# Performance work log

Measured on AMD Instinct MI355X. Metric: run time of the kernel, lower is better.

Reference implementation:

```python
import jax, jax.numpy as jnp
import numpy as np

B, T, V, D, H, C = 64, 512, 50000, 128, 256, 50


def setup_inputs() -> dict:
    key = jax.random.key(0)
    ks = jax.random.split(key, 15)
    s = 0.05
    rn = lambda k, shape: jax.random.normal(k, shape, jnp.float32) * s
    words = jax.random.randint(ks[0], (B, T), 0, V)
    target = jax.random.randint(ks[1], (B, T), 0, C)
    seq_len = jax.random.randint(ks[2], (B,), T // 2, T + 1)
    seq_len = seq_len.at[0].set(T)  # ensure at least one full-length sequence
    return dict(
        words=words, target=target, seq_len=seq_len,
        emb=rn(ks[3], (V, D)),
        W_ih_f=rn(ks[4], (4 * H, D)), W_hh_f=rn(ks[5], (4 * H, H)), b_f=rn(ks[6], (4 * H,)),
        W_ih_b=rn(ks[7], (4 * H, D)), W_hh_b=rn(ks[8], (4 * H, H)), b_b=rn(ks[9], (4 * H,)),
        fc_W=rn(ks[10], (C, 2 * H)), fc_b=rn(ks[11], (C,)),
        trans=rn(ks[12], (C, C)), start_s=rn(ks[13], (C,)), end_s=rn(ks[14], (C,)),
    )


def _lstm(x, W_ih, W_hh, b):
    # unidirectional LSTM, PyTorch gate order (i, f, g, o). x: [B,T,D] -> h: [B,T,H]
    Hh = W_hh.shape[1]
    xg = jnp.einsum('btd,gd->btg', x, W_ih) + b  # [B,T,4H]

    def step(carry, xt):
        h, c = carry
        g = xt + h @ W_hh.T
        i, f, gg, o = jnp.split(g, 4, axis=-1)
        c = jax.nn.sigmoid(f) * c + jax.nn.sigmoid(i) * jnp.tanh(gg)
        h = jax.nn.sigmoid(o) * jnp.tanh(c)
        return (h, c), h

    h0 = jnp.zeros((x.shape[0], Hh), x.dtype)
    _, hs = jax.lax.scan(step, (h0, h0), jnp.swapaxes(xg, 0, 1))
    return jnp.swapaxes(hs, 0, 1)


def _rev_idx(seq_len, t_len):
    # per-sequence time-reversal indices (packed-sequence semantics for the backward LSTM)
    t = jnp.arange(t_len)[None, :]
    L = seq_len[:, None]
    return jnp.where(t < L, L - 1 - t, t)


def _bilstm_crf_loss(words, target, seq_len, emb, W_ih_f, W_hh_f, b_f,
                     W_ih_b, W_hh_b, b_b, fc_W, fc_b, trans, start_s, end_s):
    x = emb[words]  # [B,T,D]
    h_f = _lstm(x, W_ih_f, W_hh_f, b_f)
    idx = _rev_idx(seq_len, x.shape[1])
    x_rev = jnp.take_along_axis(x, idx[:, :, None], axis=1)
    h_b = jnp.take_along_axis(_lstm(x_rev, W_ih_b, W_hh_b, b_b), idx[:, :, None], axis=1)
    feats = jnp.concatenate([h_f, h_b], axis=-1) @ fc_W.T + fc_b  # [B,T,C]
    logits = jax.nn.log_softmax(feats, axis=-1)
    mask = jnp.arange(x.shape[1])[None, :] < seq_len[:, None]  # [B,T] bool

    # --- CRF normalizer (forward algorithm) ---
    alpha0 = logits[:, 0] + start_s  # [B,C]

    def step(alpha, inp):
        emit_t, m_t = inp  # [B,C], [B]
        tmp = alpha[:, :, None] + trans[None, :, :] + emit_t[:, None, :]
        new = jax.nn.logsumexp(tmp, axis=1)
        return jnp.where(m_t[:, None], new, alpha), None

    alpha, _ = jax.lax.scan(step, alpha0,
                            (jnp.swapaxes(logits, 0, 1)[1:], jnp.swapaxes(mask, 0, 1)[1:]))
    norm = jax.nn.logsumexp(alpha + end_s, axis=1)  # [B]

    # --- gold path score ---
    maskf = mask.astype(logits.dtype)
    emit = jnp.take_along_axis(logits, target[:, :, None], axis=2)[..., 0]  # [B,T]
    trans_sc = trans[target[:, :-1], target[:, 1:]]  # [B,T-1]
    last = target[jnp.arange(target.shape[0]), seq_len - 1]
    gold = (emit * maskf).sum(1) + (trans_sc * maskf[:, 1:]).sum(1) \
           + start_s[target[:, 0]] + end_s[last]

    return jnp.mean(norm - gold)


def reference(words, target, seq_len, emb, W_ih_f, W_hh_f, b_f,
              W_ih_b, W_hh_b, b_b, fc_W, fc_b, trans, start_s, end_s):
    return _bilstm_crf_loss(words, target, seq_len, emb, W_ih_f, W_hh_f, b_f,
                            W_ih_b, W_hh_b, b_b, fc_W, fc_b, trans, start_s, end_s)
```

## Files before the change

kernel.cpp:

```cpp
#include <hip/hip_runtime.h>
#include <hip/hip_bf16.h>

#define BB 64
#define TT 512
#define DD 128
#define HH 256
#define G4 1024
#define CC 50

typedef __bf16 bf16x8 __attribute__((ext_vector_type(8)));
typedef float  f32x4  __attribute__((ext_vector_type(4)));
typedef _Float16 h16x2 __attribute__((ext_vector_type(2)));

#if defined(__has_builtin)
#if __has_builtin(__builtin_amdgcn_fdot2)
#define HAS_FDOT2 1
#endif
#endif

__device__ __forceinline__ float bl16(unsigned u) { return __uint_as_float(u << 16); }
__device__ __forceinline__ float bh16(unsigned u) { return __uint_as_float(u & 0xffff0000u); }

__device__ __forceinline__ float sigf(float x) {
    return 1.f / (1.f + __expf(-x));
}
__device__ __forceinline__ float tanh_s(float x) {
    float ax = fabsf(x);
    float e = __expf(-2.f * ax);
    float r = (1.f - e) / (1.f + e);
    return copysignf(r, x);
}

__device__ __forceinline__ float dot8(float acc, uint4 w, uint4 h) {
#ifdef HAS_FDOT2
    acc = __builtin_amdgcn_fdot2(__builtin_bit_cast(h16x2, w.x),
                                 __builtin_bit_cast(h16x2, h.x), acc, false);
    acc = __builtin_amdgcn_fdot2(__builtin_bit_cast(h16x2, w.y),
                                 __builtin_bit_cast(h16x2, h.y), acc, false);
    acc = __builtin_amdgcn_fdot2(__builtin_bit_cast(h16x2, w.z),
                                 __builtin_bit_cast(h16x2, h.z), acc, false);
    acc = __builtin_amdgcn_fdot2(__builtin_bit_cast(h16x2, w.w),
                                 __builtin_bit_cast(h16x2, h.w), acc, false);
#else
    {
        h16x2 a = __builtin_bit_cast(h16x2, w.x), b = __builtin_bit_cast(h16x2, h.x);
        acc = fmaf((float)a.x, (float)b.x, acc); acc = fmaf((float)a.y, (float)b.y, acc);
        a = __builtin_bit_cast(h16x2, w.y); b = __builtin_bit_cast(h16x2, h.y);
        acc = fmaf((float)a.x, (float)b.x, acc); acc = fmaf((float)a.y, (float)b.y, acc);
        a = __builtin_bit_cast(h16x2, w.z); b = __builtin_bit_cast(h16x2, h.z);
        acc = fmaf((float)a.x, (float)b.x, acc); acc = fmaf((float)a.y, (float)b.y, acc);
        a = __builtin_bit_cast(h16x2, w.w); b = __builtin_bit_cast(h16x2, h.w);
        acc = fmaf((float)a.x, (float)b.x, acc); acc = fmaf((float)a.y, (float)b.y, acc);
    }
#endif
    return acc;
}

__global__ __launch_bounds__(256) void k_cvt(
    const float* __restrict__ src, __hip_bfloat16* __restrict__ dst, int n)
{
    int i = (blockIdx.x * 256 + threadIdx.x) * 8;
    if (i + 8 <= n) {
        float4 a = *(const float4*)(src + i);
        float4 b = *(const float4*)(src + i + 4);
        __hip_bfloat16 o[8];
        o[0] = __float2bfloat16(a.x); o[1] = __float2bfloat16(a.y);
        o[2] = __float2bfloat16(a.z); o[3] = __float2bfloat16(a.w);
        o[4] = __float2bfloat16(b.x); o[5] = __float2bfloat16(b.y);
        o[6] = __float2bfloat16(b.z); o[7] = __float2bfloat16(b.w);
        *(uint4*)(dst + i) = *(const uint4*)o;
    }
}

__global__ __launch_bounds__(256) void k_pack(
    const float* __restrict__ Wf, const float* __restrict__ Wb,
    uint4* __restrict__ Wp)
{
    int blk = blockIdx.x;
    int g   = blk & 3;
    int kc  = (blk >> 2) & 31;
    int dir = blk >> 7;
    int j = threadIdx.x;
    int row = g * 256 + j;
    const float* src = (dir ? Wb : Wf) + (size_t)row * 256 + kc * 8;
    float4 a = *(const float4*)src;
    float4 b = *(const float4*)(src + 4);
    _Float16 o[8];
    o[0] = (_Float16)a.x; o[1] = (_Float16)a.y;
    o[2] = (_Float16)a.z; o[3] = (_Float16)a.w;
    o[4] = (_Float16)b.x; o[5] = (_Float16)b.y;
    o[6] = (_Float16)b.z; o[7] = (_Float16)b.w;
    Wp[((size_t)(dir * 32 + kc) * 4 + g) * 256 + j] = *(const uint4*)o;
}

__global__ __launch_bounds__(256, 2) void k_xg(
    const int* __restrict__ words,
    const float* __restrict__ embf,
    const __hip_bfloat16* __restrict__ Wih,
    const float* __restrict__ bfv, const float* __restrict__ bbv,
    __hip_bfloat16* __restrict__ xg)
{
    __shared__ __align__(16) __hip_bfloat16 A[64][136];
    int tid = threadIdx.x;
    int bt0 = blockIdx.x * 64;

    {
        int r = tid >> 2;
        int c0 = (tid & 3) * 32;
        int word = words[bt0 + r];
        const float* src = embf + (size_t)word * DD + c0;
#pragma unroll
        for (int i = 0; i < 8; ++i) {
            float4 v = *(const float4*)(src + i * 4);
            __hip_bfloat16 o[4] = {__float2bfloat16(v.x), __float2bfloat16(v.y),
                                   __float2bfloat16(v.z), __float2bfloat16(v.w)};
            *(uint2*)&A[r][c0 + i * 4] = *(const uint2*)o;
        }
    }
    __syncthreads();

    int wave = tid >> 6, lane = tid & 63;
    int m = lane & 15, quad = lane >> 4;

    bf16x8 afr[4][4];
#pragma unroll
    for (int ms = 0; ms < 4; ++ms)
#pragma unroll
        for (int kf = 0; kf < 4; ++kf)
            afr[ms][kf] = *(const bf16x8*)&A[ms * 16 + m][quad * 8 + kf * 32];

#pragma unroll 1
    for (int i = 0; i < 32; ++i) {
        int nt = wave * 32 + i;
        int gate_g = nt * 16 + m;
        int dir = gate_g >> 10;
        int gate = gate_g & 1023;
        const __hip_bfloat16* brow = Wih + (size_t)gate_g * DD + quad * 8;
        bf16x8 bfr[4];
#pragma unroll
        for (int kf = 0; kf < 4; ++kf) bfr[kf] = *(const bf16x8*)(brow + kf * 32);
        float bv = dir ? bbv[gate] : bfv[gate];
        size_t dbase = (size_t)dir * (size_t)(BB * TT * G4);

#pragma unroll
        for (int ms = 0; ms < 4; ++ms) {
            f32x4 acc = {0.f, 0.f, 0.f, 0.f};
#pragma unroll
            for (int kf = 0; kf < 4; ++kf)
                acc = __builtin_amdgcn_mfma_f32_16x16x32_bf16(afr[ms][kf], bfr[kf], acc, 0, 0, 0);
#pragma unroll
            for (int r = 0; r < 4; ++r) {
                int btrow = bt0 + ms * 16 + quad * 4 + r;
                xg[dbase + (size_t)btrow * G4 + gate] = __float2bfloat16(acc[r] + bv);
            }
        }
    }
}

__global__ __launch_bounds__(512)
__attribute__((amdgpu_waves_per_eu(2, 2)))
void k_lstm(
    const __hip_bfloat16* __restrict__ xg,
    const uint4* __restrict__ Wp,
    const int* __restrict__ seq_len,
    __hip_bfloat16* __restrict__ hcat)
{
    int b = blockIdx.x & 63;
    int dir = blockIdx.x >> 6;
    int tid = threadIdx.x;
    int j   = tid & 255;
    int half = tid >> 8;

    __shared__ __align__(16) uint4 wlds[16 * 512];
    __shared__ __align__(16) _Float16 hbf[2][HH];
    __shared__ float pbuf[4][HH];

    const uint4* Wd = Wp + (size_t)dir * (32 * 4 * 256);

    uint4 wr[12][4];
#pragma unroll
    for (int kcl = 0; kcl < 12; ++kcl)
#pragma unroll
        for (int g = 0; g < 4; ++g)
            wr[kcl][g] = Wd[(((kcl + 16 * half) * 4 + g) * 256) + j];

#pragma unroll
    for (int kcl = 12; kcl < 16; ++kcl)
#pragma unroll
        for (int g = 0; g < 4; ++g)
            wlds[((kcl - 12) * 4 + g) * 512 + tid] =
                Wd[(((kcl + 16 * half) * 4 + g) * 256) + j];

    if (half == 0) hbf[0][j] = (_Float16)0.f;
    float c = 0.f;
    int L = seq_len[b];
    const __hip_bfloat16* xgb = xg + (size_t)dir * (size_t)(BB * TT * G4)
                                   + (size_t)b * TT * G4;

    int tc = dir ? (L - 1) : 0;
    float xv0 = 0.f, xv1 = 0.f, xv2 = 0.f, xv3 = 0.f;
    if (half == 0) {
        const __hip_bfloat16* xr = xgb + (size_t)tc * G4 + j;
        xv0 = __bfloat162float(xr[0]);   xv1 = __bfloat162float(xr[256]);
        xv2 = __bfloat162float(xr[512]); xv3 = __bfloat162float(xr[768]);
    }
    __syncthreads();

#pragma unroll 1
    for (int t = 0; t < TT; ++t) {
#pragma unroll
        for (int kcl = 0; kcl < 12; ++kcl)
#pragma unroll
            for (int g = 0; g < 4; ++g)
                asm volatile("" : "+v"(wr[kcl][g].x), "+v"(wr[kcl][g].y),
                                  "+v"(wr[kcl][g].z), "+v"(wr[kcl][g].w));

        int cur = t & 1, nxt = cur ^ 1;
        int tn = t + 1;
        int tcn = dir ? ((tn < L) ? (L - 1 - tn) : tn) : tn;
        bool pf = (tn < TT);
        __hip_bfloat16 p0, p1, p2, p3;
        if (half == 0 && pf) {
            const __hip_bfloat16* xr = xgb + (size_t)tcn * G4 + j;
            p0 = xr[0]; p1 = xr[256]; p2 = xr[512]; p3 = xr[768];
        }

        unsigned off = 0;
        asm volatile("" : "+v"(off));

        const _Float16* hrow = &hbf[cur][half * 128];
        float a0 = 0.f, a1 = 0.f, a2 = 0.f, a3 = 0.f;
#pragma unroll
        for (int kcl = 0; kcl < 12; ++kcl) {
            uint4 hv = *(const uint4*)(hrow + kcl * 8);
            a0 = dot8(a0, wr[kcl][0], hv);
            a1 = dot8(a1, wr[kcl][1], hv);
            a2 = dot8(a2, wr[kcl][2], hv);
            a3 = dot8(a3, wr[kcl][3], hv);
        }
#pragma unroll
        for (int kcl = 12; kcl < 16; ++kcl) {
            uint4 hv = *(const uint4*)(hrow + kcl * 8);
            int m0 = (kcl - 12) * 4;
            uint4 w0 = wlds[(m0 + 0) * 512 + tid + off];
            uint4 w1 = wlds[(m0 + 1) * 512 + tid + off];
            uint4 w2 = wlds[(m0 + 2) * 512 + tid + off];
            uint4 w3 = wlds[(m0 + 3) * 512 + tid + off];
            a0 = dot8(a0, w0, hv);
            a1 = dot8(a1, w1, hv);
            a2 = dot8(a2, w2, hv);
            a3 = dot8(a3, w3, hv);
            __builtin_amdgcn_sched_barrier(0);
        }

        if (half) {
            pbuf[0][j] = a0; pbuf[1][j] = a1;
            pbuf[2][j] = a2; pbuf[3][j] = a3;
        }
        __syncthreads();

        if (half == 0) {
            float gi = a0 + pbuf[0][j] + xv0;
            float gf = a1 + pbuf[1][j] + xv1;
            float gg = a2 + pbuf[2][j] + xv2;
            float go = a3 + pbuf[3][j] + xv3;
            float i_ = sigf(gi), f_ = sigf(gf), G = tanh_s(gg), o_ = sigf(go);
            c = f_ * c + i_ * G;
            float h = o_ * tanh_s(c);
            hbf[nxt][j] = (_Float16)h;
            hcat[((size_t)(b * TT + tc)) * (2 * HH) + dir * HH + j] = __float2bfloat16(h);
            if (pf) {
                xv0 = __bfloat162float(p0); xv1 = __bfloat162float(p1);
                xv2 = __bfloat162float(p2); xv3 = __bfloat162float(p3);
            }
        }
        tc = tcn;
        __syncthreads();
    }
}

__global__ __launch_bounds__(64) void k_fc(
    const __hip_bfloat16* __restrict__ hcat,
    const __hip_bfloat16* __restrict__ fcW,
    const float* __restrict__ fcb,
    float* __restrict__ logits)
{
    int row = blockIdx.x;
    int tid = threadIdx.x;
    __shared__ __align__(16) float hrow[2 * HH];
    __shared__ float fbuf[CC + 2];

    {
        uint4 v = *(const uint4*)(hcat + (size_t)row * (2 * HH) + tid * 8);
        float* d = &hrow[tid * 8];
        d[0] = bl16(v.x); d[1] = bh16(v.x);
        d[2] = bl16(v.y); d[3] = bh16(v.y);
        d[4] = bl16(v.z); d[5] = bh16(v.z);
        d[6] = bl16(v.w); d[7] = bh16(v.w);
    }
    __syncthreads();

    if (tid < CC) {
        float acc = fcb[tid];
        const uint4* wr = (const uint4*)(fcW + (size_t)tid * (2 * HH));
#pragma unroll 8
        for (int kc = 0; kc < 64; ++kc) {
            uint4 wv = wr[kc];
            float4 h0 = *(const float4*)&hrow[kc * 8];
            float4 h1 = *(const float4*)&hrow[kc * 8 + 4];
            acc = fmaf(bl16(wv.x), h0.x, acc); acc = fmaf(bh16(wv.x), h0.y, acc);
            acc = fmaf(bl16(wv.y), h0.z, acc); acc = fmaf(bh16(wv.y), h0.w, acc);
            acc = fmaf(bl16(wv.z), h1.x, acc); acc = fmaf(bh16(wv.z), h1.y, acc);
            acc = fmaf(bl16(wv.w), h1.z, acc); acc = fmaf(bh16(wv.w), h1.w, acc);
        }
        fbuf[tid] = acc;
    }
    __syncthreads();

    float m = -1e30f;
    for (int i = 0; i < CC; ++i) m = fmaxf(m, fbuf[i]);
    float s = 0.f;
    for (int i = 0; i < CC; ++i) s += __expf(fbuf[i] - m);
    float lns = __logf(s);
    if (tid < CC) logits[(size_t)row * CC + tid] = fbuf[tid] - m - lns;
}

__global__ __launch_bounds__(256) void k_crf(
    const float* __restrict__ logits,
    const int* __restrict__ target,
    const int* __restrict__ seq_len,
    const float* __restrict__ trans,
    const float* __restrict__ start_s,
    const float* __restrict__ end_s,
    float* __restrict__ loss_b)
{
    const float L2E = 1.4426950408889634f;
    const float LN2 = 0.6931471805599453f;
    int b = blockIdx.x;
    int tid = threadIdx.x;
    int q = tid >> 6;
    int j = tid & 63;
    bool act = (j < CC);
    int L = seq_len[b];
    const float* lg = logits + (size_t)b * TT * CC;

    __shared__ float alpha2[64];
    __shared__ float mpart[4][64];
    __shared__ float spart[4][64];
    __shared__ float red[256];
    __shared__ float nbuf[CC + 2];

    int i0 = q * 13;
    int icnt = min(13, CC - i0);
    float treg[13];
    if (act) {
#pragma unroll
        for (int s = 0; s < 13; ++s)
            if (s < icnt) treg[s] = L2E * trans[(i0 + s) * CC + j];
    }
    if (q == 0 && act) alpha2[j] = L2E * (lg[j] + start_s[j]);
    __syncthreads();

    float v[13];
    for (int t = 1; t < L; ++t) {
        float mq = -1e30f;
        if (act) {
#pragma unroll
            for (int s = 0; s < 13; ++s)
                if (s < icnt) { v[s] = alpha2[i0 + s] + treg[s]; mq = fmaxf(mq, v[s]); }
        }
        mpart[q][j] = mq;
        __syncthreads();
        float M = fmaxf(fmaxf(mpart[0][j], mpart[1][j]), fmaxf(mpart[2][j], mpart[3][j]));
        float sq = 0.f;
        if (act) {
#pragma unroll
            for (int s = 0; s < 13; ++s)
                if (s < icnt) sq += exp2f(v[s] - M);
        }
        spart[q][j] = sq;
        __syncthreads();
        if (q == 0 && act) {
            float S = spart[0][j] + spart[1][j] + spart[2][j] + spart[3][j];
            alpha2[j] = M + log2f(S) + L2E * lg[(size_t)t * CC + j];
        }
        __syncthreads();
    }

    if (q == 0 && act) nbuf[j] = alpha2[j] + L2E * end_s[j];

    float gp = 0.f;
    const int* tg = target + b * TT;
    for (int t = tid; t < TT; t += 256) {
        if (t < L) {
            int c = tg[t];
            gp += lg[(size_t)t * CC + c];
            if (t >= 1) gp += trans[tg[t - 1] * CC + c];
        }
    }
    red[tid] = gp;
    __syncthreads();

    if (tid == 0) {
        float m2 = -1e30f;
        for (int i = 0; i < CC; ++i) m2 = fmaxf(m2, nbuf[i]);
        float s2 = 0.f;
        for (int i = 0; i < CC; ++i) s2 += exp2f(nbuf[i] - m2);
        float norm_nat = (m2 + log2f(s2)) * LN2;
        float g = 0.f;
        for (int i = 0; i < 256; ++i) g += red[i];
        g += start_s[tg[0]] + end_s[tg[L - 1]];
        loss_b[b] = norm_nat - g;
    }
}

__global__ void k_fin(const float* __restrict__ loss_b, float* __restrict__ out)
{
    int t = threadIdx.x;
    float v = loss_b[t];
#pragma unroll
    for (int o = 32; o > 0; o >>= 1) v += __shfl_down(v, o);
    if (t == 0) out[0] = v * (1.f / BB);
}

extern "C" void kernel_launch(void* const* d_in, const int* in_sizes, int n_in,
                              void* d_out, int out_size, void* d_ws, size_t ws_size,
                              hipStream_t stream)
{
    const int* words   = (const int*)d_in[0];
    const int* target  = (const int*)d_in[1];
    const int* seq_len = (const int*)d_in[2];
    const float* emb    = (const float*)d_in[3];
    const float* W_ih_f = (const float*)d_in[4];
    const float* W_hh_f = (const float*)d_in[5];
    const float* b_f    = (const float*)d_in[6];
    const float* W_ih_b = (const float*)d_in[7];
    const float* W_hh_b = (const float*)d_in[8];
    const float* b_b    = (const float*)d_in[9];
    const float* fc_W   = (const float*)d_in[10];
    const float* fc_b   = (const float*)d_in[11];
    const float* trans  = (const float*)d_in[12];
    const float* start_s= (const float*)d_in[13];
    const float* end_s  = (const float*)d_in[14];

    char* ws = (char*)d_ws;
    __hip_bfloat16* xg     = (__hip_bfloat16*)ws;
    __hip_bfloat16* hcat   = (__hip_bfloat16*)(ws + 134217728);
    float*          logits = (float*)(ws + 167772160);
    uint4*          Wp     = (uint4*)(ws + 167772160);
    float*          loss_b = (float*)(ws + 174325760);
    __hip_bfloat16* wihall = (__hip_bfloat16*)(ws + 174326016);
    __hip_bfloat16* fcw_bf = (__hip_bfloat16*)(ws + 174850304);

    k_cvt<<<64,  256, 0, stream>>>(W_ih_f, wihall,          131072);
    k_cvt<<<64,  256, 0, stream>>>(W_ih_b, wihall + 131072, 131072);
    k_cvt<<<13,  256, 0, stream>>>(fc_W,   fcw_bf,          25600);
    k_pack<<<256, 256, 0, stream>>>(W_hh_f, W_hh_b, Wp);

    k_xg  <<<512, 256, 0, stream>>>(words, emb, wihall, b_f, b_b, xg);
    k_lstm<<<128, 512, 0, stream>>>(xg, Wp, seq_len, hcat);
    k_fc  <<<32768, 64, 0, stream>>>(hcat, fcw_bf, fc_b, logits);
    k_crf <<<64, 256, 0, stream>>>(logits, target, seq_len, trans, start_s, end_s, loss_b);
    k_fin <<<1, 64, 0, stream>>>(loss_b, (float*)d_out);
}
```

Before: 1.796 ms.

## Stream LSTM recurrent weights from global memory and batch FC rows per block

The LSTM kernel stops keeping 12 weight chunks per thread resident in registers. It keeps only 2 in registers and 4 in LDS, and reloads the other 10 chunks from global/L2 every timestep through a double-buffered software prefetch. This frees registers but adds a large amount of per-step global memory traffic on the serial recurrence path. Separately, the FC/log-softmax kernel now handles four rows per 256-thread block instead of one row per 64-thread block, which cuts the block count.

New measurement: 2.609 ms. 45.3% more time.

```diff
diff --git a/kernel.cpp b/kernel.cpp
--- a/kernel.cpp
+++ b/kernel.cpp
@@ -157,8 +157,18 @@
     }
 }
 
-__global__ __launch_bounds__(512)
-__attribute__((amdgpu_waves_per_eu(2, 2)))
+#define GLOAD(BUF, P) {                                   \
+    BUF[0] = *(const uint4*)((P));                        \
+    BUF[1] = *(const uint4*)((P) + 4096);                 \
+    BUF[2] = *(const uint4*)((P) + 8192);                 \
+    BUF[3] = *(const uint4*)((P) + 12288); }
+
+#define CONSUME(K, W0, W1, W2, W3) {                      \
+    uint4 hv = *(const uint4*)(hrow + (K) * 8);           \
+    a0 = dot8(a0, W0, hv); a1 = dot8(a1, W1, hv);         \
+    a2 = dot8(a2, W2, hv); a3 = dot8(a3, W3, hv); }
+
+__global__ __launch_bounds__(512, 2)
 void k_lstm(
     const __hip_bfloat16* __restrict__ xg,
     const uint4* __restrict__ Wp,
@@ -177,12 +187,12 @@
 
     const uint4* Wd = Wp + (size_t)dir * (32 * 4 * 256);
 
-    uint4 wr[12][4];
-#pragma unroll
-    for (int kcl = 0; kcl < 12; ++kcl)
+    uint4 wh[2][4];
+#pragma unroll
+    for (int kcl = 0; kcl < 2; ++kcl)
 #pragma unroll
         for (int g = 0; g < 4; ++g)
-            wr[kcl][g] = Wd[(((kcl + 16 * half) * 4 + g) * 256) + j];
+            wh[kcl][g] = Wd[(((kcl + 16 * half) * 4 + g) * 256) + j];
 
 #pragma unroll
     for (int kcl = 12; kcl < 16; ++kcl)
@@ -190,6 +200,14 @@
         for (int g = 0; g < 4; ++g)
             wlds[((kcl - 12) * 4 + g) * 512 + tid] =
                 Wd[(((kcl + 16 * half) * 4 + g) * 256) + j];
+
+    const char* Wbase = (const char*)Wd
+                      + ((size_t)(16 * half) * 4) * 4096 + (size_t)j * 16;
+    const char* pA = Wbase + 2 * 16384;
+    const char* pB = Wbase + 3 * 16384;
+    uint4 sA[4], sB[4];
+    GLOAD(sA, pA); pA += 32768;
+    GLOAD(sB, pB); pB += 32768;
 
     if (half == 0) hbf[0][j] = (_Float16)0.f;
     float c = 0.f;
@@ -209,11 +227,17 @@
 #pragma unroll 1
     for (int t = 0; t < TT; ++t) {
 #pragma unroll
-        for (int kcl = 0; kcl < 12; ++kcl)
+        for (int kcl = 0; kcl < 2; ++kcl)
 #pragma unroll
             for (int g = 0; g < 4; ++g)
-                asm volatile("" : "+v"(wr[kcl][g].x), "+v"(wr[kcl][g].y),
-                                  "+v"(wr[kcl][g].z), "+v"(wr[kcl][g].w));
+                asm volatile("" : "+v"(wh[kcl][g].x), "+v"(wh[kcl][g].y),
+                                  "+v"(wh[kcl][g].z), "+v"(wh[kcl][g].w));
+        {
+            unsigned long long uA = (unsigned long long)pA;
+            unsigned long long uB = (unsigned long long)pB;
+            asm volatile("" : "+v"(uA), "+v"(uB));
+            pA = (const char*)uA; pB = (const char*)uB;
+        }
 
         int cur = t & 1, nxt = cur ^ 1;
         int tn = t + 1;
@@ -225,32 +249,35 @@
             p0 = xr[0]; p1 = xr[256]; p2 = xr[512]; p3 = xr[768];
         }
 
-        unsigned off = 0;
-        asm volatile("" : "+v"(off));
-
         const _Float16* hrow = &hbf[cur][half * 128];
         float a0 = 0.f, a1 = 0.f, a2 = 0.f, a3 = 0.f;
-#pragma unroll
-        for (int kcl = 0; kcl < 12; ++kcl) {
-            uint4 hv = *(const uint4*)(hrow + kcl * 8);
-            a0 = dot8(a0, wr[kcl][0], hv);
-            a1 = dot8(a1, wr[kcl][1], hv);
-            a2 = dot8(a2, wr[kcl][2], hv);
-            a3 = dot8(a3, wr[kcl][3], hv);
-        }
+
+        CONSUME(0, wh[0][0], wh[0][1], wh[0][2], wh[0][3]);
+        CONSUME(1, wh[1][0], wh[1][1], wh[1][2], wh[1][3]);
+
+        CONSUME(2, sA[0], sA[1], sA[2], sA[3]); GLOAD(sA, pA); pA += 32768;
+        CONSUME(3, sB[0], sB[1], sB[2], sB[3]); GLOAD(sB, pB); pB += 32768;
+        CONSUME(4, sA[0], sA[1], sA[2], sA[3]); GLOAD(sA, pA); pA += 32768;
+        CONSUME(5, sB[0], sB[1], sB[2], sB[3]); GLOAD(sB, pB); pB += 32768;
+        CONSUME(6, sA[0], sA[1], sA[2], sA[3]); GLOAD(sA, pA); pA += 32768;
+        CONSUME(7, sB[0], sB[1], sB[2], sB[3]); GLOAD(sB, pB); pB += 32768;
+        CONSUME(8, sA[0], sA[1], sA[2], sA[3]); GLOAD(sA, pA); pA += 32768 - 163840;
+        CONSUME(9, sB[0], sB[1], sB[2], sB[3]); GLOAD(sB, pB); pB += 32768 - 163840;
+        CONSUME(10, sA[0], sA[1], sA[2], sA[3]); GLOAD(sA, pA); pA += 32768;
+        CONSUME(11, sB[0], sB[1], sB[2], sB[3]); GLOAD(sB, pB); pB += 32768;
+
 #pragma unroll
         for (int kcl = 12; kcl < 16; ++kcl) {
             uint4 hv = *(const uint4*)(hrow + kcl * 8);
             int m0 = (kcl - 12) * 4;
-            uint4 w0 = wlds[(m0 + 0) * 512 + tid + off];
-            uint4 w1 = wlds[(m0 + 1) * 512 + tid + off];
-            uint4 w2 = wlds[(m0 + 2) * 512 + tid + off];
-            uint4 w3 = wlds[(m0 + 3) * 512 + tid + off];
+            uint4 w0 = wlds[(m0 + 0) * 512 + tid];
+            uint4 w1 = wlds[(m0 + 1) * 512 + tid];
+            uint4 w2 = wlds[(m0 + 2) * 512 + tid];
+            uint4 w3 = wlds[(m0 + 3) * 512 + tid];
             a0 = dot8(a0, w0, hv);
             a1 = dot8(a1, w1, hv);
             a2 = dot8(a2, w2, hv);
             a3 = dot8(a3, w3, hv);
-            __builtin_amdgcn_sched_barrier(0);
         }
 
         if (half) {
@@ -279,20 +306,21 @@
     }
 }
 
-__global__ __launch_bounds__(64) void k_fc(
+__global__ __launch_bounds__(256) void k_fc(
     const __hip_bfloat16* __restrict__ hcat,
     const __hip_bfloat16* __restrict__ fcW,
     const float* __restrict__ fcb,
     float* __restrict__ logits)
 {
-    int row = blockIdx.x;
-    int tid = threadIdx.x;
-    __shared__ __align__(16) float hrow[2 * HH];
-    __shared__ float fbuf[CC + 2];
+    int team = threadIdx.x >> 6;
+    int tid  = threadIdx.x & 63;
+    int row  = blockIdx.x * 4 + team;
+    __shared__ __align__(16) float hrow[4][2 * HH];
+    __shared__ float fbuf[4][CC + 2];
 
     {
         uint4 v = *(const uint4*)(hcat + (size_t)row * (2 * HH) + tid * 8);
-        float* d = &hrow[tid * 8];
+        float* d = &hrow[team][tid * 8];
         d[0] = bl16(v.x); d[1] = bh16(v.x);
         d[2] = bl16(v.y); d[3] = bh16(v.y);
         d[4] = bl16(v.z); d[5] = bh16(v.z);
@@ -306,23 +334,23 @@
 #pragma unroll 8
         for (int kc = 0; kc < 64; ++kc) {
             uint4 wv = wr[kc];
-            float4 h0 = *(const float4*)&hrow[kc * 8];
-            float4 h1 = *(const float4*)&hrow[kc * 8 + 4];
+            float4 h0 = *(const float4*)&hrow[team][kc * 8];
+            float4 h1 = *(const float4*)&hrow[team][kc * 8 + 4];
             acc = fmaf(bl16(wv.x), h0.x, acc); acc = fmaf(bh16(wv.x), h0.y, acc);
             acc = fmaf(bl16(wv.y), h0.z, acc); acc = fmaf(bh16(wv.y), h0.w, acc);
             acc = fmaf(bl16(wv.z), h1.x, acc); acc = fmaf(bh16(wv.z), h1.y, acc);
             acc = fmaf(bl16(wv.w), h1.z, acc); acc = fmaf(bh16(wv.w), h1.w, acc);
         }
-        fbuf[tid] = acc;
+        fbuf[team][tid] = acc;
     }
     __syncthreads();
 
     float m = -1e30f;
-    for (int i = 0; i < CC; ++i) m = fmaxf(m, fbuf[i]);
+    for (int i = 0; i < CC; ++i) m = fmaxf(m, fbuf[team][i]);
     float s = 0.f;
-    for (int i = 0; i < CC; ++i) s += __expf(fbuf[i] - m);
+    for (int i = 0; i < CC; ++i) s += __expf(fbuf[team][i] - m);
     float lns = __logf(s);
-    if (tid < CC) logits[(size_t)row * CC + tid] = fbuf[tid] - m - lns;
+    if (tid < CC) logits[(size_t)row * CC + tid] = fbuf[team][tid] - m - lns;
 }
 
 __global__ __launch_bounds__(256) void k_crf(
@@ -459,7 +487,7 @@
 
     k_xg  <<<512, 256, 0, stream>>>(words, emb, wihall, b_f, b_b, xg);
     k_lstm<<<128, 512, 0, stream>>>(xg, Wp, seq_len, hcat);
-    k_fc  <<<32768, 64, 0, stream>>>(hcat, fcw_bf, fc_b, logits);
+    k_fc  <<<8192, 256, 0, stream>>>(hcat, fcw_bf, fc_b, logits);
     k_crf <<<64, 256, 0, stream>>>(logits, target, seq_len, trans, start_s, end_s, loss_b);
     k_fin <<<1, 64, 0, stream>>>(loss_b, (float*)d_out);
 }
```
